# Performance work log

Hardware: AMD Instinct MI355X
Metric: run time of the kernel (lower is better)

Reference implementation:

```python
import jax, jax.numpy as jnp
import numpy as np

B, T, D = 1, 4096, 1024
H = 16
HEAD_DIM = D // H
WINDOW = 256


def setup_inputs() -> dict:
    key = jax.random.key(0)
    k1, k2, k3 = jax.random.split(key, 3)
    x = jax.random.normal(k1, (B, T, D), dtype=jnp.float32)
    # torch nn.Linear(D, 3D) weight is (3D, D); we store transposed (D, 3D) for x @ W
    w_qkv = jax.random.normal(k2, (D, 3 * D), dtype=jnp.float32) * (1.0 / np.sqrt(D))
    w_out = jax.random.normal(k3, (D, D), dtype=jnp.float32) * (1.0 / np.sqrt(D))
    return {"x": x, "w_qkv": w_qkv, "w_out": w_out}


def reference(x, w_qkv, w_out):
    b, t, d = x.shape
    qkv = x @ w_qkv                                   # (B, T, 3D)
    q, k, v = jnp.split(qkv, 3, axis=-1)
    def split_heads(a):                               # (B, T, D) -> (B, H, T, dh)
        return a.reshape(b, t, H, HEAD_DIM).transpose(0, 2, 1, 3)
    q, k, v = split_heads(q), split_heads(k), split_heads(v)
    scale = jnp.sqrt(jnp.float32(HEAD_DIM))
    scores = jnp.einsum('bhqd,bhkd->bhqk', q, k) / scale   # (B, H, T, T)
    rows = jnp.arange(t)[:, None]
    cols = jnp.arange(t)[None, :]
    # causal sliding window: j <= i and j >= i - window + 1
    mask = (cols <= rows) & (cols >= rows - WINDOW + 1)     # (T, T) bool
    scores = jnp.where(mask[None, None], scores, -jnp.inf)
    attn = jax.nn.softmax(scores, axis=-1)
    out = jnp.einsum('bhqk,bhkd->bhqd', attn, v)            # (B, H, T, dh)
    out = out.transpose(0, 2, 1, 3).reshape(b, t, d)        # merge heads
    return out @ w_out
```

## Files before the change

### kernel.cpp

```cpp
#include <hip/hip_runtime.h>
#include <hip/hip_bf16.h>

#define T_SEQ 4096
#define DMODEL 1024
#define NH 16
#define DH 64
#define N_QKV 3072

typedef __attribute__((ext_vector_type(8))) short bf16x8;
typedef __attribute__((ext_vector_type(4))) float f32x4;

__device__ inline void gload_lds16(const __hip_bfloat16* g, __hip_bfloat16* l) {
  __builtin_amdgcn_global_load_lds(
      (const __attribute__((address_space(1))) void*)g,
      (__attribute__((address_space(3))) void*)l, 16, 0, 0);
}

__global__ void cast_x_kernel(const float* __restrict__ in,
                              __hip_bfloat16* __restrict__ out, int n) {
  int i = (blockIdx.x * 256 + threadIdx.x) * 4;
  if (i >= n) return;
  float4 v = *(const float4*)(in + i);
  ushort4 o;
  o.x = __bfloat16_as_ushort(__float2bfloat16(v.x));
  o.y = __bfloat16_as_ushort(__float2bfloat16(v.y));
  o.z = __bfloat16_as_ushort(__float2bfloat16(v.z));
  o.w = __bfloat16_as_ushort(__float2bfloat16(v.w));
  *(ushort4*)((unsigned short*)out + i) = o;
}

__global__ void transpose_cast_kernel(const float* __restrict__ in,
                                      __hip_bfloat16* __restrict__ out,
                                      int NN, int KK) {
  __shared__ float tile[32][33];
  int bn = blockIdx.x * 32, bk = blockIdx.y * 32;
  int tx = threadIdx.x & 31, ty = threadIdx.x >> 5;
#pragma unroll
  for (int r = 0; r < 32; r += 8)
    tile[ty + r][tx] = in[(size_t)(bk + ty + r) * NN + bn + tx];
  __syncthreads();
#pragma unroll
  for (int r = 0; r < 32; r += 8)
    out[(size_t)(bn + ty + r) * KK + bk + tx] = __float2bfloat16(tile[tx][ty + r]);
}

__global__ void transpose_v_kernel(const __hip_bfloat16* __restrict__ qkv,
                                   __hip_bfloat16* __restrict__ vt) {
  __shared__ unsigned short tile[32][33];
  int c0 = blockIdx.x * 32;
  int t0 = blockIdx.y * 32;
  int tx = threadIdx.x & 31, ty = threadIdx.x >> 5;
  const unsigned short* in = (const unsigned short*)qkv;
  unsigned short* out = (unsigned short*)vt;
#pragma unroll
  for (int r = 0; r < 32; r += 8)
    tile[ty + r][tx] = in[(size_t)(t0 + ty + r) * N_QKV + 2 * DMODEL + c0 + tx];
  __syncthreads();
#pragma unroll
  for (int r = 0; r < 32; r += 8)
    out[(size_t)(c0 + ty + r) * T_SEQ + t0 + tx] = tile[tx][ty + r];
}

__global__ __launch_bounds__(512, 2) void gemm8_qkv(
    const __hip_bfloat16* __restrict__ A, const __hip_bfloat16* __restrict__ Bt,
    __hip_bfloat16* __restrict__ C) {
  const int K = DMODEL;
  const int N = N_QKV;
  __shared__ alignas(16) __hip_bfloat16 Ab[4][256 * 32];
  __shared__ alignas(16) __hip_bfloat16 Bb[4][256 * 32];

  const int tid = threadIdx.x;
  const int lane = tid & 63;
  const int w = tid >> 6;
  const int wr = w >> 2, wc = w & 3;
  const int frow = lane & 15, fgrp = lane >> 4;

  const int nblk = N >> 8;
  const int cpx = (gridDim.x) >> 3;
  const int bid = blockIdx.x;
  const int sbid = (bid & 7) * cpx + (bid >> 3);
  const int mb = sbid / nblk, nb = sbid % nblk;
  const int brow = mb << 8, bcol = nb << 8;

  const int rr = w * 16 + (lane >> 2);
  const int swzc = ((lane & 3) ^ ((rr >> 1) & 3)) << 3;
  const __hip_bfloat16* aA0 = A + (size_t)(brow + rr) * K + swzc;
  const __hip_bfloat16* aA1 = A + (size_t)(brow + 128 + rr) * K + swzc;
  const __hip_bfloat16* aB0 = Bt + (size_t)(bcol + rr) * K + swzc;
  const __hip_bfloat16* aB1 = Bt + (size_t)(bcol + 128 + rr) * K + swzc;
  const int dstOff0 = (w * 16) * 32;
  const int dstOff1 = (128 + w * 16) * 32;

  f32x4 acc[8][4] = {};

#pragma unroll
  for (int t = 0; t < 3; t++) {
    gload_lds16(aA0 + t * 32, &Ab[t][dstOff0]);
    gload_lds16(aA1 + t * 32, &Ab[t][dstOff1]);
    gload_lds16(aB0 + t * 32, &Bb[t][dstOff0]);
    gload_lds16(aB1 + t * 32, &Bb[t][dstOff1]);
  }

  for (int g = 0; g < 32; ++g) {
    if (g <= 29)
      asm volatile("s_waitcnt vmcnt(8)" ::: "memory");
    else if (g == 30)
      asm volatile("s_waitcnt vmcnt(4)" ::: "memory");
    else
      asm volatile("s_waitcnt vmcnt(0)" ::: "memory");
    __builtin_amdgcn_s_barrier();

    const __hip_bfloat16* As = Ab[g & 3];
    const __hip_bfloat16* Bs = Bb[g & 3];
    bf16x8 bfr[4], af[8];

#pragma unroll
    for (int n = 0; n < 4; n++) {
      int row = wc * 64 + n * 16 + frow;
      bfr[n] = *(const bf16x8*)(Bs + row * 32 + ((fgrp ^ ((row >> 1) & 3)) << 3));
    }
#pragma unroll
    for (int m = 0; m < 8; m++) {
      int row = wr * 128 + m * 16 + frow;
      af[m] = *(const bf16x8*)(As + row * 32 + ((fgrp ^ ((row >> 1) & 3)) << 3));
    }
    if (g <= 28) {
      int t = g + 3;
      gload_lds16(aA0 + t * 32, &Ab[t & 3][dstOff0]);
      gload_lds16(aA1 + t * 32, &Ab[t & 3][dstOff1]);
      gload_lds16(aB0 + t * 32, &Bb[t & 3][dstOff0]);
      gload_lds16(aB1 + t * 32, &Bb[t & 3][dstOff1]);
    }
    __builtin_amdgcn_s_barrier();
    __builtin_amdgcn_s_setprio(1);
#pragma unroll
    for (int m = 0; m < 8; m++)
#pragma unroll
      for (int n = 0; n < 4; n++)
        acc[m][n] = __builtin_amdgcn_mfma_f32_16x16x32_bf16(af[m], bfr[n], acc[m][n], 0, 0, 0);
    __builtin_amdgcn_s_setprio(0);
  }

  const int orow0 = brow + wr * 128 + 4 * fgrp;
  const int ocol0 = bcol + wc * 64 + frow;
#pragma unroll
  for (int m = 0; m < 8; m++)
#pragma unroll
    for (int n = 0; n < 4; n++) {
      int col = ocol0 + n * 16;
      float sc = (col < DMODEL) ? 0.125f : 1.0f;
#pragma unroll
      for (int j = 0; j < 4; j++) {
        int row = orow0 + m * 16 + j;
        C[(size_t)row * N + col] = __float2bfloat16(acc[m][n][j] * sc);
      }
    }
}

__global__ __launch_bounds__(256) void gemm_out(
    const __hip_bfloat16* __restrict__ A, const __hip_bfloat16* __restrict__ Bt,
    float* __restrict__ C) {
  const int K = DMODEL, N = DMODEL;
  __shared__ alignas(16) __hip_bfloat16 Ab[4][128 * 32];
  __shared__ alignas(16) __hip_bfloat16 Bb[4][64 * 32];
  const int tid = threadIdx.x, lane = tid & 63, w = tid >> 6;
  const int wr = w >> 1, wc = w & 1;
  const int frow = lane & 15, fgrp = lane >> 4;
  const int bid = blockIdx.x;
  const int sbid = (bid & 7) * 64 + (bid >> 3);
  const int mb = sbid >> 4, nb = sbid & 15;
  const int brow = mb * 128, bcol = nb * 64;

  const int rrA = w * 32 + (lane >> 2);
  const int swzA = ((lane & 3) ^ ((rrA >> 1) & 3)) << 3;
  const int rrB = w * 16 + (lane >> 2);
  const int swzB = ((lane & 3) ^ ((rrB >> 1) & 3)) << 3;
  const __hip_bfloat16* aA0 = A + (size_t)(brow + rrA) * K + swzA;
  const __hip_bfloat16* aB0 = Bt + (size_t)(bcol + rrB) * K + swzB;
  const int dA0 = (w * 32) * 32, dA1 = (w * 32 + 16) * 32, dB0 = (w * 16) * 32;

  f32x4 acc[4][2] = {};
#pragma unroll
  for (int t = 0; t < 3; t++) {
    gload_lds16(aA0 + t * 32, &Ab[t][dA0]);
    gload_lds16(aA0 + 16 * (size_t)K + t * 32, &Ab[t][dA1]);
    gload_lds16(aB0 + t * 32, &Bb[t][dB0]);
  }
  for (int g = 0; g < 32; ++g) {
    if (g <= 29)
      asm volatile("s_waitcnt vmcnt(6)" ::: "memory");
    else if (g == 30)
      asm volatile("s_waitcnt vmcnt(3)" ::: "memory");
    else
      asm volatile("s_waitcnt vmcnt(0)" ::: "memory");
    __builtin_amdgcn_s_barrier();
    const __hip_bfloat16* As = Ab[g & 3];
    const __hip_bfloat16* Bs = Bb[g & 3];
    bf16x8 af[4], bfr[2];
#pragma unroll
    for (int m = 0; m < 4; m++) {
      int row = wr * 64 + m * 16 + frow;
      af[m] = *(const bf16x8*)(As + row * 32 + ((fgrp ^ ((row >> 1) & 3)) << 3));
    }
#pragma unroll
    for (int n = 0; n < 2; n++) {
      int row = wc * 32 + n * 16 + frow;
      bfr[n] = *(const bf16x8*)(Bs + row * 32 + ((fgrp ^ ((row >> 1) & 3)) << 3));
    }
    if (g <= 28) {
      int t = g + 3;
      gload_lds16(aA0 + t * 32, &Ab[t & 3][dA0]);
      gload_lds16(aA0 + 16 * (size_t)K + t * 32, &Ab[t & 3][dA1]);
      gload_lds16(aB0 + t * 32, &Bb[t & 3][dB0]);
    }
    __builtin_amdgcn_s_barrier();
    __builtin_amdgcn_s_setprio(1);
#pragma unroll
    for (int m = 0; m < 4; m++)
#pragma unroll
      for (int n = 0; n < 2; n++)
        acc[m][n] = __builtin_amdgcn_mfma_f32_16x16x32_bf16(af[m], bfr[n], acc[m][n], 0, 0, 0);
    __builtin_amdgcn_s_setprio(0);
  }
  const int orow0 = brow + wr * 64 + 4 * fgrp;
  const int ocol0 = bcol + wc * 32 + frow;
#pragma unroll
  for (int m = 0; m < 4; m++)
#pragma unroll
    for (int n = 0; n < 2; n++)
#pragma unroll
      for (int j = 0; j < 4; j++)
        C[(size_t)(orow0 + m * 16 + j) * N + ocol0 + n * 16] = acc[m][n][j];
}

__global__ __launch_bounds__(256) void swa_kernel(
    const __hip_bfloat16* __restrict__ qkv, const __hip_bfloat16* __restrict__ vt,
    __hip_bfloat16* __restrict__ attn_out) {
  const int b = blockIdx.x;
  const int s = (b & 7) * 128 + (b >> 3);
  const int h = s >> 6;
  const int qb = s & 63;
  const int tid = threadIdx.x;
  const int lane = tid & 63;
  const int w = tid >> 6;
  const int frow = lane & 15;
  const int fgrp = lane >> 4;
  const int fk = fgrp * 8;

  __shared__ alignas(16) __hip_bfloat16 Ks[2][64 * 64];
  __shared__ alignas(16) __hip_bfloat16 Vs[2][64 * 64];
  __shared__ alignas(16) __hip_bfloat16 Pl[4][16 * 72];

  const int qrow_g = qb * 64 + w * 16 + frow;
  bf16x8 aq[2];
  {
    const __hip_bfloat16* qptr = qkv + (size_t)qrow_g * N_QKV + h * DH;
    aq[0] = *(const bf16x8*)(qptr + fk);
    aq[1] = *(const bf16x8*)(qptr + 32 + fk);
  }

  f32x4 o[4] = {};
  float l_run[4] = {0.f, 0.f, 0.f, 0.f};

  const int srow = lane >> 3;
  const int ssw = (((lane & 7) ^ srow) << 3);
  const __hip_bfloat16* kbase =
      qkv + (size_t)(w * 16 + srow) * N_QKV + DMODEL + h * DH + ssw;
  const __hip_bfloat16* vbase =
      vt + (size_t)(h * DH + w * 16 + srow) * T_SEQ + ssw;

  const int kb0 = qb >= 4 ? qb - 4 : 0;

  {
    const __hip_bfloat16* ks = kbase + (size_t)kb0 * 64 * N_QKV;
    gload_lds16(ks, &Ks[0][w * 16 * 64]);
    gload_lds16(ks + 8 * (size_t)N_QKV, &Ks[0][(w * 16 + 8) * 64]);
    const __hip_bfloat16* vs = vbase + kb0 * 64;
    gload_lds16(vs, &Vs[0][w * 16 * 64]);
    gload_lds16(vs + 8 * (size_t)T_SEQ, &Vs[0][(w * 16 + 8) * 64]);
  }

  for (int kb = kb0; kb <= qb; kb++) {
    const int buf = (kb - kb0) & 1;
    if (kb < qb) {
      const __hip_bfloat16* ks = kbase + (size_t)(kb + 1) * 64 * N_QKV;
      gload_lds16(ks, &Ks[buf ^ 1][w * 16 * 64]);
      gload_lds16(ks + 8 * (size_t)N_QKV, &Ks[buf ^ 1][(w * 16 + 8) * 64]);
      const __hip_bfloat16* vs = vbase + (kb + 1) * 64;
      gload_lds16(vs, &Vs[buf ^ 1][w * 16 * 64]);
      gload_lds16(vs + 8 * (size_t)T_SEQ, &Vs[buf ^ 1][(w * 16 + 8) * 64]);
      asm volatile("s_waitcnt vmcnt(4)" ::: "memory");
    } else {
      asm volatile("s_waitcnt vmcnt(0)" ::: "memory");
    }
    __builtin_amdgcn_s_barrier();

    f32x4 sc[4];
#pragma unroll
    for (int n = 0; n < 4; n++) sc[n] = (f32x4){0.f, 0.f, 0.f, 0.f};
#pragma unroll
    for (int n = 0; n < 4; n++) {
      int rowk = n * 16 + frow;
      int x = rowk & 7;
      bf16x8 bk0 = *(const bf16x8*)(&Ks[buf][rowk * 64 + ((fgrp ^ x) << 3)]);
      bf16x8 bk1 = *(const bf16x8*)(&Ks[buf][rowk * 64 + (((4 + fgrp) ^ x) << 3)]);
      sc[n] = __builtin_amdgcn_mfma_f32_16x16x32_bf16(aq[0], bk0, sc[n], 0, 0, 0);
      sc[n] = __builtin_amdgcn_mfma_f32_16x16x32_bf16(aq[1], bk1, sc[n], 0, 0, 0);
    }

    const bool edge_hi = (kb == qb);
    const bool edge_lo = (kb == qb - 4);
#pragma unroll
    for (int r = 0; r < 4; r++) {
      const int row_l = w * 16 + 4 * fgrp + r;
      float rs = 0.f;
#pragma unroll
      for (int n = 0; n < 4; n++) {
        int col_l = n * 16 + frow;
        bool valid = (!edge_hi || col_l <= row_l) && (!edge_lo || col_l > row_l);
        float p = valid ? __expf(sc[n][r]) : 0.f;
        sc[n][r] = p;
        rs += p;
      }
      l_run[r] += rs;
    }

    __hip_bfloat16* pw = &Pl[w][0];
#pragma unroll
    for (int n = 0; n < 4; n++)
#pragma unroll
      for (int r = 0; r < 4; r++)
        pw[(4 * fgrp + r) * 72 + n * 16 + frow] = __float2bfloat16(sc[n][r]);

#pragma unroll
    for (int c = 0; c < 2; c++) {
      bf16x8 ap = *(const bf16x8*)(pw + frow * 72 + c * 32 + fk);
#pragma unroll
      for (int nd = 0; nd < 4; nd++) {
        int rowd = nd * 16 + frow;
        int x = rowd & 7;
        bf16x8 bv = *(const bf16x8*)(&Vs[buf][rowd * 64 + (((c * 4 + fgrp) ^ x) << 3)]);
        o[nd] = __builtin_amdgcn_mfma_f32_16x16x32_bf16(ap, bv, o[nd], 0, 0, 0);
      }
    }
    __builtin_amdgcn_s_barrier();
  }

#pragma unroll
  for (int r = 0; r < 4; r++) {
    float l = l_run[r];
    l += __shfl_xor(l, 1);
    l += __shfl_xor(l, 2);
    l += __shfl_xor(l, 4);
    l += __shfl_xor(l, 8);
    l_run[r] = l;
  }
#pragma unroll
  for (int nd = 0; nd < 4; nd++)
#pragma unroll
    for (int r = 0; r < 4; r++) {
      float v = o[nd][r] / l_run[r];
      attn_out[(size_t)(qb * 64 + w * 16 + 4 * fgrp + r) * DMODEL + h * DH + nd * 16 + frow] =
          __float2bfloat16(v);
    }
}

extern "C" void kernel_launch(void* const* d_in, const int* in_sizes, int n_in,
                              void* d_out, int out_size, void* d_ws, size_t ws_size,
                              hipStream_t stream) {
  const float* x = (const float*)d_in[0];
  const float* w_qkv = (const float*)d_in[1];
  const float* w_out = (const float*)d_in[2];
  float* out = (float*)d_out;

  char* ws = (char*)d_ws;
  __hip_bfloat16* x_bf = (__hip_bfloat16*)ws;
  __hip_bfloat16* vt = (__hip_bfloat16*)ws;
  __hip_bfloat16* wqkvT = (__hip_bfloat16*)(ws + 8388608);
  __hip_bfloat16* woutT = (__hip_bfloat16*)(ws + 14680064);
  __hip_bfloat16* qkv_bf = (__hip_bfloat16*)(ws + 16777216);
  __hip_bfloat16* attn_bf = (__hip_bfloat16*)(ws + 41943040);

  cast_x_kernel<<<4096, 256, 0, stream>>>(x, x_bf, T_SEQ * DMODEL);
  transpose_cast_kernel<<<dim3(N_QKV / 32, DMODEL / 32), 256, 0, stream>>>(w_qkv, wqkvT, N_QKV, DMODEL);
  transpose_cast_kernel<<<dim3(DMODEL / 32, DMODEL / 32), 256, 0, stream>>>(w_out, woutT, DMODEL, DMODEL);

  gemm8_qkv<<<(T_SEQ / 256) * (N_QKV / 256), 512, 0, stream>>>(x_bf, wqkvT, qkv_bf);

  transpose_v_kernel<<<dim3(DMODEL / 32, T_SEQ / 32), 256, 0, stream>>>(qkv_bf, vt);

  swa_kernel<<<(T_SEQ / 64) * NH, 256, 0, stream>>>(qkv_bf, vt, attn_bf);

  gemm_out<<<512, 256, 0, stream>>>(attn_bf, woutT, out);
}
```

Measured before the change: 92.10 us.

## Retile QKV GEMM to 256x192 tiles with K=64 stages and split A pipeline

Changes the QKV projection GEMM tile from 256x256 to 256x192, which raises the grid from 192 to 256 blocks so it matches the CU count better. K steps double to 64, with 8-slot XOR swizzling. A gets a triple buffer and B a double buffer. Each K step is split into two halves so the second half of A fragments and the next A prefetch overlap the first half of the MFMAs. Per-block reuse drops a little, and the kernel adds an extra barrier per iteration plus a different LDS footprint, which could affect occupancy.

```diff
diff --git a/kernel.cpp b/kernel.cpp
--- a/kernel.cpp
+++ b/kernel.cpp
@@ -66,8 +66,8 @@
     __hip_bfloat16* __restrict__ C) {
   const int K = DMODEL;
   const int N = N_QKV;
-  __shared__ alignas(16) __hip_bfloat16 Ab[4][256 * 32];
-  __shared__ alignas(16) __hip_bfloat16 Bb[4][256 * 32];
+  __shared__ alignas(16) __hip_bfloat16 Ab[3][256 * 64];
+  __shared__ alignas(16) __hip_bfloat16 Bb[2][192 * 64];
 
   const int tid = threadIdx.x;
   const int lane = tid & 63;
@@ -75,78 +75,110 @@
   const int wr = w >> 2, wc = w & 3;
   const int frow = lane & 15, fgrp = lane >> 4;
 
-  const int nblk = N >> 8;
-  const int cpx = (gridDim.x) >> 3;
   const int bid = blockIdx.x;
-  const int sbid = (bid & 7) * cpx + (bid >> 3);
-  const int mb = sbid / nblk, nb = sbid % nblk;
-  const int brow = mb << 8, bcol = nb << 8;
-
-  const int rr = w * 16 + (lane >> 2);
-  const int swzc = ((lane & 3) ^ ((rr >> 1) & 3)) << 3;
-  const __hip_bfloat16* aA0 = A + (size_t)(brow + rr) * K + swzc;
-  const __hip_bfloat16* aA1 = A + (size_t)(brow + 128 + rr) * K + swzc;
-  const __hip_bfloat16* aB0 = Bt + (size_t)(bcol + rr) * K + swzc;
-  const __hip_bfloat16* aB1 = Bt + (size_t)(bcol + 128 + rr) * K + swzc;
-  const int dstOff0 = (w * 16) * 32;
-  const int dstOff1 = (128 + w * 16) * 32;
-
-  f32x4 acc[8][4] = {};
-
-#pragma unroll
-  for (int t = 0; t < 3; t++) {
-    gload_lds16(aA0 + t * 32, &Ab[t][dstOff0]);
-    gload_lds16(aA1 + t * 32, &Ab[t][dstOff1]);
-    gload_lds16(aB0 + t * 32, &Bb[t][dstOff0]);
-    gload_lds16(aB1 + t * 32, &Bb[t][dstOff1]);
-  }
-
-  for (int g = 0; g < 32; ++g) {
-    if (g <= 29)
-      asm volatile("s_waitcnt vmcnt(8)" ::: "memory");
-    else if (g == 30)
+  const int sbid = (bid & 7) * 32 + (bid >> 3);
+  const int mb = sbid >> 4, nb = sbid & 15;
+  const int brow = mb << 8, bcol = nb * 192;
+
+  const int srow = lane >> 3;
+  const int sslot = (lane & 7) ^ srow;
+  const __hip_bfloat16* aSrcA = A + (size_t)(brow + w * 32 + srow) * K + sslot * 8;
+  const __hip_bfloat16* aSrcB = Bt + (size_t)(bcol + w * 24 + srow) * K + sslot * 8;
+  const int dstA = (w * 32 + srow) * 64 + (lane & 7) * 8;
+  const int dstB = (w * 24 + srow) * 64 + (lane & 7) * 8;
+
+  f32x4 acc[8][3] = {};
+
+#pragma unroll
+  for (int i = 0; i < 4; i++)
+    gload_lds16(aSrcA + (size_t)(i * 8) * K, &Ab[0][dstA + i * 8 * 64]);
+#pragma unroll
+  for (int i = 0; i < 3; i++)
+    gload_lds16(aSrcB + (size_t)(i * 8) * K, &Bb[0][dstB + i * 8 * 64]);
+#pragma unroll
+  for (int i = 0; i < 4; i++)
+    gload_lds16(aSrcA + (size_t)(i * 8) * K + 64, &Ab[1][dstA + i * 8 * 64]);
+
+  for (int t = 0; t < 16; ++t) {
+    if (t < 15)
       asm volatile("s_waitcnt vmcnt(4)" ::: "memory");
     else
       asm volatile("s_waitcnt vmcnt(0)" ::: "memory");
     __builtin_amdgcn_s_barrier();
 
-    const __hip_bfloat16* As = Ab[g & 3];
-    const __hip_bfloat16* Bs = Bb[g & 3];
-    bf16x8 bfr[4], af[8];
-
-#pragma unroll
-    for (int n = 0; n < 4; n++) {
-      int row = wc * 64 + n * 16 + frow;
-      bfr[n] = *(const bf16x8*)(Bs + row * 32 + ((fgrp ^ ((row >> 1) & 3)) << 3));
-    }
-#pragma unroll
-    for (int m = 0; m < 8; m++) {
+    const __hip_bfloat16* As = &Ab[t % 3][0];
+    const __hip_bfloat16* Bs = &Bb[t & 1][0];
+    bf16x8 bfrag[3][2], afrag[4][2];
+
+#pragma unroll
+    for (int n = 0; n < 3; n++) {
+      int row = wc * 48 + n * 16 + frow;
+#pragma unroll
+      for (int kh = 0; kh < 2; kh++) {
+        int slot = (kh * 4 + fgrp) ^ (row & 7);
+        bfrag[n][kh] = *(const bf16x8*)(Bs + row * 64 + slot * 8);
+      }
+    }
+#pragma unroll
+    for (int m = 0; m < 4; m++) {
       int row = wr * 128 + m * 16 + frow;
-      af[m] = *(const bf16x8*)(As + row * 32 + ((fgrp ^ ((row >> 1) & 3)) << 3));
-    }
-    if (g <= 28) {
-      int t = g + 3;
-      gload_lds16(aA0 + t * 32, &Ab[t & 3][dstOff0]);
-      gload_lds16(aA1 + t * 32, &Ab[t & 3][dstOff1]);
-      gload_lds16(aB0 + t * 32, &Bb[t & 3][dstOff0]);
-      gload_lds16(aB1 + t * 32, &Bb[t & 3][dstOff1]);
+#pragma unroll
+      for (int kh = 0; kh < 2; kh++) {
+        int slot = (kh * 4 + fgrp) ^ (row & 7);
+        afrag[m][kh] = *(const bf16x8*)(As + row * 64 + slot * 8);
+      }
+    }
+    if (t + 1 < 16) {
+      __hip_bfloat16* bd = &Bb[(t + 1) & 1][0];
+#pragma unroll
+      for (int i = 0; i < 3; i++)
+        gload_lds16(aSrcB + (size_t)(i * 8) * K + (t + 1) * 64, bd + dstB + i * 8 * 64);
     }
     __builtin_amdgcn_s_barrier();
     __builtin_amdgcn_s_setprio(1);
 #pragma unroll
-    for (int m = 0; m < 8; m++)
-#pragma unroll
-      for (int n = 0; n < 4; n++)
-        acc[m][n] = __builtin_amdgcn_mfma_f32_16x16x32_bf16(af[m], bfr[n], acc[m][n], 0, 0, 0);
+    for (int m = 0; m < 4; m++)
+#pragma unroll
+      for (int n = 0; n < 3; n++) {
+        acc[m][n] = __builtin_amdgcn_mfma_f32_16x16x32_bf16(afrag[m][0], bfrag[n][0], acc[m][n], 0, 0, 0);
+        acc[m][n] = __builtin_amdgcn_mfma_f32_16x16x32_bf16(afrag[m][1], bfrag[n][1], acc[m][n], 0, 0, 0);
+      }
     __builtin_amdgcn_s_setprio(0);
+    __builtin_amdgcn_s_barrier();
+
+#pragma unroll
+    for (int m = 0; m < 4; m++) {
+      int row = wr * 128 + (m + 4) * 16 + frow;
+#pragma unroll
+      for (int kh = 0; kh < 2; kh++) {
+        int slot = (kh * 4 + fgrp) ^ (row & 7);
+        afrag[m][kh] = *(const bf16x8*)(As + row * 64 + slot * 8);
+      }
+    }
+    if (t + 2 < 16) {
+      __hip_bfloat16* ad = &Ab[(t + 2) % 3][0];
+#pragma unroll
+      for (int i = 0; i < 4; i++)
+        gload_lds16(aSrcA + (size_t)(i * 8) * K + (t + 2) * 64, ad + dstA + i * 8 * 64);
+    }
+    __builtin_amdgcn_s_barrier();
+    __builtin_amdgcn_s_setprio(1);
+#pragma unroll
+    for (int m = 0; m < 4; m++)
+#pragma unroll
+      for (int n = 0; n < 3; n++) {
+        acc[m + 4][n] = __builtin_amdgcn_mfma_f32_16x16x32_bf16(afrag[m][0], bfrag[n][0], acc[m + 4][n], 0, 0, 0);
+        acc[m + 4][n] = __builtin_amdgcn_mfma_f32_16x16x32_bf16(afrag[m][1], bfrag[n][1], acc[m + 4][n], 0, 0, 0);
+      }
+    __builtin_amdgcn_s_setprio(0);
   }
 
   const int orow0 = brow + wr * 128 + 4 * fgrp;
-  const int ocol0 = bcol + wc * 64 + frow;
+  const int ocol0 = bcol + wc * 48 + frow;
 #pragma unroll
   for (int m = 0; m < 8; m++)
 #pragma unroll
-    for (int n = 0; n < 4; n++) {
+    for (int n = 0; n < 3; n++) {
       int col = ocol0 + n * 16;
       float sc = (col < DMODEL) ? 0.125f : 1.0f;
 #pragma unroll
@@ -385,7 +417,7 @@
   transpose_cast_kernel<<<dim3(N_QKV / 32, DMODEL / 32), 256, 0, stream>>>(w_qkv, wqkvT, N_QKV, DMODEL);
   transpose_cast_kernel<<<dim3(DMODEL / 32, DMODEL / 32), 256, 0, stream>>>(w_out, woutT, DMODEL, DMODEL);
 
-  gemm8_qkv<<<(T_SEQ / 256) * (N_QKV / 256), 512, 0, stream>>>(x_bf, wqkvT, qkv_bf);
+  gemm8_qkv<<<(T_SEQ / 256) * (N_QKV / 192), 512, 0, stream>>>(x_bf, wqkvT, qkv_bf);
 
   transpose_v_kernel<<<dim3(DMODEL / 32, T_SEQ / 32), 256, 0, stream>>>(qkv_bf, vt);
 
```

Result: faster. 85.82 us (-6.8%).
